# Kernel optimization log

Measured on AMD Instinct MI355X. Metric: run time of the kernel, lower is better.

Reference implementation:

```python
import jax, jax.numpy as jnp
import numpy as np

# Dims: C = 8*8*4 = 256 input channels, O = 8*8*8 = 512 output channels,
# space_rank = 4, TT ranks = (4, 16, 16).

def setup_inputs() -> dict:
    key = jax.random.key(0)
    ks = jax.random.split(key, 6)
    inp = jax.random.normal(ks[0], (32, 256, 32, 32), dtype=jnp.float32)
    # space_factor: (space_rank, 1, kH, kW)
    space_factor = jax.random.normal(ks[1], (4, 1, 3, 3), dtype=jnp.float32) * 0.3
    # factors[i]: (in_i, rank_i, rank_{i+1}, out_i)
    factor0 = jax.random.normal(ks[2], (8, 4, 16, 8), dtype=jnp.float32) * 0.1
    factor1 = jax.random.normal(ks[3], (8, 16, 16, 8), dtype=jnp.float32) * 0.08
    # last_factor: (in_last, rank_last, out_last)
    last_factor = jax.random.normal(ks[4], (4, 16, 8), dtype=jnp.float32) * 0.1
    bias = jax.random.uniform(ks[5], (512,), dtype=jnp.float32, minval=-0.02, maxval=0.02)
    return {"input": inp, "space_factor": space_factor, "factor0": factor0,
            "factor1": factor1, "last_factor": last_factor, "bias": bias}


def reference(input, space_factor, factor0, factor1, last_factor, bias):
    B, C, H, W = input.shape
    sr = space_factor.shape[0]
    # Depthwise conv: each of the C channels convolved with the same
    # `space_rank` filters (torch repeat along out-channel dim + groups=C).
    w = jnp.tile(space_factor, (C, 1, 1, 1))  # (C*sr, 1, kH, kW)
    y = jax.lax.conv_general_dilated(
        input, w, window_strides=(1, 1), padding=[(1, 1), (1, 1)],
        feature_group_count=C,
        dimension_numbers=("NCHW", "OIHW", "NCHW"))  # (B, C*sr, H', W')
    Hp, Wp = y.shape[2], y.shape[3]
    # (B, n0, n1, n2, sr, H', W') with (n0,n1,n2) = input_chanel_shape
    t = y.reshape(B, 8, 8, 4, sr, Hp, Wp)
    # Contract the tiny TT cores first (optimal order found by tn.contractors.optimal):
    # chain: (n0, n1, n2, r0, o0, o1, o2) -- only ~0.5M elements.
    chain = jnp.einsum("apqx,bqry,crz->abcpxyz", factor0, factor1, last_factor)
    # One big contraction over (n0, n1, n2, r0): effectively a GEMM
    # (B*H'*W', C*sr) x (C*sr, O).
    out = jnp.einsum("nabcphw,abcpxyz->nxyzhw", t, chain)
    out = out.reshape(B, 512, Hp, Wp)
    return out + bias[None, :, None, None]
```

## Files before the change

kernel.cpp:

```cpp
#include <hip/hip_runtime.h>

typedef unsigned short ushort_t;
typedef __attribute__((ext_vector_type(8))) short bf16x8;
typedef __attribute__((ext_vector_type(4))) float f32x4;

__device__ __forceinline__ unsigned short f2bf(float f) {
  union { float f; unsigned u; } x; x.f = f;
  unsigned r = x.u + 0x7FFFu + ((x.u >> 16) & 1u);
  return (unsigned short)(r >> 16);
}

__global__ void chain_g_kernel(const float* __restrict__ f1,
                               const float* __restrict__ lf,
                               float* __restrict__ g) {
  int idx = blockIdx.x * 256 + threadIdx.x;
  int z = idx & 7, c = (idx >> 3) & 3, y = (idx >> 5) & 7,
      q = (idx >> 8) & 15, b = idx >> 12;
  float s = 0.f;
  #pragma unroll
  for (int r = 0; r < 16; ++r)
    s += f1[((b * 16 + q) * 16 + r) * 8 + y] * lf[(c * 16 + r) * 8 + z];
  g[idx] = s;
}

__global__ void chain_kernel(const float* __restrict__ f0,
                             const float* __restrict__ g,
                             ushort_t* __restrict__ chainT) {
  int idx = blockIdx.x * 256 + threadIdx.x;
  int k = idx & 1023, o = idx >> 10;
  int p = k & 3, c = (k >> 2) & 3, b = (k >> 4) & 7, a = k >> 7;
  int z = o & 7, y = (o >> 3) & 7, x = o >> 6;
  float s = 0.f;
  #pragma unroll
  for (int q = 0; q < 16; ++q)
    s += f0[((a * 4 + p) * 16 + q) * 8 + x] *
         g[(((b * 16 + q) * 8 + y) * 4 + c) * 8 + z];
  chainT[idx] = f2bf(s);
}

#define AS1 __attribute__((address_space(1)))
#define AS3 __attribute__((address_space(3)))
#define BARRIER  __builtin_amdgcn_s_barrier()
#define LGKMCNT0 asm volatile("s_waitcnt lgkmcnt(0)" ::: "memory")
#define VMCNT3   asm volatile("s_waitcnt vmcnt(3)" ::: "memory")
#define VMCNT0   asm volatile("s_waitcnt vmcnt(0)" ::: "memory")

__global__ __launch_bounds__(512, 2) void fused_kernel(const float* __restrict__ in,
                                                       const float* __restrict__ sf,
                                                       const ushort_t* __restrict__ chainT,
                                                       const float* __restrict__ bias,
                                                       float* __restrict__ out) {
  __shared__ __align__(16) ushort_t Bs[32768];
  __shared__ __align__(16) ushort_t As[2][8192];
  __shared__ __align__(16) float Is[6528];

  int tid = threadIdx.x;
  int bid = blockIdx.x;
  int wg = (bid & 7) * 32 + (bid >> 3);
  int n = wg >> 3, hq = wg & 7;
  int h0 = hq * 4;

  int lane = tid & 63, wv = tid >> 6;
  int wm = (wv >> 2) * 64, wn = (wv & 3) * 128;
  int lr = lane & 15, kg = lane >> 4;
  int kph0 = ((kg * 8) ^ ((lane & 7) * 8));
  int kph1 = ((32 + kg * 8) ^ ((lane & 7) * 8));

  int srow = tid >> 3;
  int scol = ((tid & 7) ^ (srow & 7)) * 8;
  const ushort_t* sB = chainT + (size_t)srow * 1024 + scol;

  int cw = tid & 31, hp = (tid >> 5) & 1, ch2 = wv;
  int clm = (cw == 0) ? 33 : cw - 1;
  int crp = (cw == 31) ? 32 : cw + 1;
  int aswz = (ch2 ^ (cw & 7)) * 8;

  int isrc[3], ild[3], izer[3];
  #pragma unroll
  for (int i = 0; i < 3; ++i) {
    int e = tid + i * 512;
    int ch = e / 96, rem = e % 96, r = rem >> 4, w2 = rem & 15;
    int hh = h0 - 1 + r;
    int hcl = hh < 0 ? 0 : (hh > 31 ? 31 : hh);
    izer[i] = (hh < 0) | (hh > 31);
    isrc[i] = ch * 1024 + hcl * 32 + w2 * 2;
    ild[i]  = ch * 204 + r * 34 + w2 * 2;
  }
  const float* inb = in + (size_t)n * 262144;
  float2 rin[3];

  float sfr[36];
  #pragma unroll
  for (int i = 0; i < 36; ++i)
    sfr[i] = __int_as_float(__builtin_amdgcn_readfirstlane(__float_as_int(sf[i])));

  float bv[8];
  #pragma unroll
  for (int nf = 0; nf < 8; ++nf) bv[nf] = bias[wn + nf * 16 + lr];

  f32x4 acc[4][8];
  #pragma unroll
  for (int i = 0; i < 4; ++i)
    #pragma unroll
    for (int j = 0; j < 8; ++j) acc[i][j] = (f32x4){0.f, 0.f, 0.f, 0.f};

#define ISSUE_IN(KT)                                                                     \
  _Pragma("unroll")                                                                      \
  for (int i = 0; i < 3; ++i)                                                            \
    rin[i] = *(const float2*)&inb[(size_t)(KT) * 16384 + isrc[i]];

#define WRITE_IN(IB)                                                                     \
  _Pragma("unroll")                                                                      \
  for (int i = 0; i < 3; ++i) {                                                          \
    float2 v = rin[i];                                                                   \
    if (izer[i]) { v.x = 0.f; v.y = 0.f; }                                               \
    *(float2*)&Is[(IB) * 3264 + ild[i]] = v;                                             \
  }

#define STAGE_B(KT)                                                                      \
  _Pragma("unroll")                                                                      \
  for (int l = 0; l < 8; ++l)                                                            \
    __builtin_amdgcn_global_load_lds(                                                    \
        (const AS1 void*)(sB + (size_t)l * 65536 + (KT) * 64),                           \
        (AS3 void*)&Bs[l * 4096 + tid * 8], 16, 0, 0);

#define CONV(IB, AB)                                                                     \
  {                                                                                      \
    float tap[2][4][3];                                                                  \
    _Pragma("unroll")                                                                    \
    for (int b = 0; b < 2; ++b) {                                                        \
      const float* isp = &Is[(IB) * 3264 + (ch2 * 2 + b) * 204];                         \
      _Pragma("unroll")                                                                  \
      for (int r4 = 0; r4 < 4; ++r4) {                                                   \
        int rb = (hp * 2 + r4) * 34;                                                     \
        tap[b][r4][0] = isp[rb + clm];                                                   \
        tap[b][r4][1] = isp[rb + cw];                                                    \
        tap[b][r4][2] = isp[rb + crp];                                                   \
      }                                                                                  \
    }                                                                                    \
    _Pragma("unroll")                                                                    \
    for (int j = 0; j < 2; ++j) {                                                        \
      unsigned pw[4];                                                                    \
      _Pragma("unroll")                                                                  \
      for (int b = 0; b < 2; ++b) {                                                      \
        float s[4];                                                                      \
        _Pragma("unroll")                                                                \
        for (int p = 0; p < 4; ++p) {                                                    \
          float a_ = 0.f;                                                                \
          _Pragma("unroll")                                                              \
          for (int dr = 0; dr < 3; ++dr)                                                 \
            _Pragma("unroll")                                                            \
            for (int dt = 0; dt < 3; ++dt)                                               \
              a_ += tap[b][j + dr][dt] * sfr[p * 9 + dr * 3 + dt];                       \
          s[p] = a_;                                                                     \
        }                                                                                \
        pw[b * 2 + 0] = (unsigned)f2bf(s[0]) | ((unsigned)f2bf(s[1]) << 16);             \
        pw[b * 2 + 1] = (unsigned)f2bf(s[2]) | ((unsigned)f2bf(s[3]) << 16);             \
      }                                                                                  \
      uint4 pk; pk.x = pw[0]; pk.y = pw[1]; pk.z = pw[2]; pk.w = pw[3];                  \
      int row = (hp * 2 + j) * 32 + cw;                                                  \
      *(uint4*)&As[AB][row * 64 + aswz] = pk;                                            \
    }                                                                                    \
  }

#define MFMA_PHASE(AB)                                                                   \
  _Pragma("unroll")                                                                      \
  for (int ks = 0; ks < 2; ++ks) {                                                       \
    int kph = ks ? kph1 : kph0;                                                          \
    bf16x8 af[4];                                                                        \
    _Pragma("unroll")                                                                    \
    for (int mf = 0; mf < 4; ++mf)                                                       \
      af[mf] = *(const bf16x8*)&As[AB][(wm + mf * 16 + lr) * 64 + kph];                  \
    _Pragma("unroll")                                                                    \
    for (int ng = 0; ng < 2; ++ng) {                                                     \
      bf16x8 bq[4];                                                                      \
      _Pragma("unroll")                                                                  \
      for (int nq = 0; nq < 4; ++nq)                                                     \
        bq[nq] = *(const bf16x8*)&Bs[(wn + ng * 64 + nq * 16 + lr) * 64 + kph];          \
      __builtin_amdgcn_s_setprio(1);                                                     \
      _Pragma("unroll")                                                                  \
      for (int mf = 0; mf < 4; ++mf)                                                     \
        _Pragma("unroll")                                                                \
        for (int nq = 0; nq < 4; ++nq)                                                   \
          acc[mf][ng * 4 + nq] = __builtin_amdgcn_mfma_f32_16x16x32_bf16(                \
              af[mf], bq[nq], acc[mf][ng * 4 + nq], 0, 0, 0);                            \
      __builtin_amdgcn_s_setprio(0);                                                     \
    }                                                                                    \
  }

  if (tid < 384) {
    int bb = tid / 192, rem = tid % 192, ch = rem / 12, rr = rem % 12;
    Is[bb * 3264 + ch * 204 + (rr >> 1) * 34 + 32 + (rr & 1)] = 0.f;
  }
  ISSUE_IN(0)
  WRITE_IN(0)
  ISSUE_IN(1)
  LGKMCNT0; BARRIER;
  CONV(0, 0)
  WRITE_IN(1)
  STAGE_B(0)
  ISSUE_IN(2)
  LGKMCNT0; VMCNT3; BARRIER;

  #pragma unroll 1
  for (int I = 0; I < 8; ++I) {
    MFMA_PHASE(0)
    CONV(1, 1)
    if (I < 7) { WRITE_IN(0) }
    LGKMCNT0; BARRIER;
    STAGE_B(2 * I + 1)
    if (I < 7) { ISSUE_IN(2 * I + 3) VMCNT3; } else { VMCNT0; }
    BARRIER;
    MFMA_PHASE(1)
    if (I < 7) { CONV(0, 0) WRITE_IN(1) }
    LGKMCNT0; BARRIER;
    if (I < 7) {
      STAGE_B(2 * I + 2)
      if (I < 6) { ISSUE_IN(2 * I + 4) VMCNT3; } else { VMCNT0; }
    }
    BARRIER;
  }

  #pragma unroll
  for (int mf = 0; mf < 4; ++mf)
    #pragma unroll
    for (int nf = 0; nf < 8; ++nf) {
      int mloc = hq * 128 + wm + mf * 16 + kg * 4;
      int o = wn + nf * 16 + lr;
      f32x4 vv = acc[mf][nf];
      vv[0] += bv[nf]; vv[1] += bv[nf]; vv[2] += bv[nf]; vv[3] += bv[nf];
      *(f32x4*)&out[(size_t)n * 524288 + (size_t)o * 1024 + mloc] = vv;
    }
}

extern "C" void kernel_launch(void* const* d_in, const int* in_sizes, int n_in,
                              void* d_out, int out_size, void* d_ws, size_t ws_size,
                              hipStream_t stream) {
  (void)in_sizes; (void)n_in; (void)out_size; (void)ws_size;
  const float* in   = (const float*)d_in[0];
  const float* sf   = (const float*)d_in[1];
  const float* f0   = (const float*)d_in[2];
  const float* f1   = (const float*)d_in[3];
  const float* lf   = (const float*)d_in[4];
  const float* bias = (const float*)d_in[5];
  float* out = (float*)d_out;

  char* ws = (char*)d_ws;
  ushort_t* chainT = (ushort_t*)ws;
  float*    g      = (float*)(ws + 1048576);

  hipLaunchKernelGGL(chain_g_kernel, dim3(128),  dim3(256), 0, stream, f1, lf, g);
  hipLaunchKernelGGL(chain_kernel,   dim3(2048), dim3(256), 0, stream, f0, g, chainT);
  hipLaunchKernelGGL(fused_kernel,   dim3(256),  dim3(512), 0, stream, in, sf, chainT, bias, out);
}
```

Baseline: 74.21 us.

## Split output channels across two workgroups to raise occupancy and grid size

Each workgroup now computes half of the 512 output channels, so the grid doubles to 512 blocks and the accumulator and B tile shrink by half. Launch bounds ask for 4 blocks per CU, and the input staging buffer is single-buffered and unpadded, with edge zeros handled in registers. This is meant to fill the 256 CUs better and hide latency with more resident waves. In exchange the depthwise conv is recomputed twice per pixel tile, there are more barriers per iteration, and the single input buffer serializes conv and staging.

```diff
diff --git a/kernel.cpp b/kernel.cpp
--- a/kernel.cpp
+++ b/kernel.cpp
@@ -45,34 +45,32 @@
 #define VMCNT3   asm volatile("s_waitcnt vmcnt(3)" ::: "memory")
 #define VMCNT0   asm volatile("s_waitcnt vmcnt(0)" ::: "memory")
 
-__global__ __launch_bounds__(512, 2) void fused_kernel(const float* __restrict__ in,
+__global__ __launch_bounds__(512, 4) void fused_kernel(const float* __restrict__ in,
                                                        const float* __restrict__ sf,
                                                        const ushort_t* __restrict__ chainT,
                                                        const float* __restrict__ bias,
                                                        float* __restrict__ out) {
-  __shared__ __align__(16) ushort_t Bs[32768];
+  __shared__ __align__(16) ushort_t Bs[16384];
   __shared__ __align__(16) ushort_t As[2][8192];
-  __shared__ __align__(16) float Is[6528];
+  __shared__ __align__(16) float Is[3072];
 
   int tid = threadIdx.x;
   int bid = blockIdx.x;
-  int wg = (bid & 7) * 32 + (bid >> 3);
-  int n = wg >> 3, hq = wg & 7;
-  int h0 = hq * 4;
+  int wg = (bid & 7) * 64 + (bid >> 3);
+  int pix = wg >> 1, nh = wg & 1;
+  int n = pix >> 3, hq = pix & 7, h0 = hq * 4;
 
   int lane = tid & 63, wv = tid >> 6;
-  int wm = (wv >> 2) * 64, wn = (wv & 3) * 128;
+  int wm = (wv >> 2) * 64, wn = (wv & 3) * 64;
   int lr = lane & 15, kg = lane >> 4;
   int kph0 = ((kg * 8) ^ ((lane & 7) * 8));
   int kph1 = ((32 + kg * 8) ^ ((lane & 7) * 8));
 
   int srow = tid >> 3;
   int scol = ((tid & 7) ^ (srow & 7)) * 8;
-  const ushort_t* sB = chainT + (size_t)srow * 1024 + scol;
+  const ushort_t* sB = chainT + (size_t)(nh * 256 + srow) * 1024 + scol;
 
   int cw = tid & 31, hp = (tid >> 5) & 1, ch2 = wv;
-  int clm = (cw == 0) ? 33 : cw - 1;
-  int crp = (cw == 31) ? 32 : cw + 1;
   int aswz = (ch2 ^ (cw & 7)) * 8;
 
   int isrc[3], ild[3], izer[3];
@@ -84,7 +82,7 @@
     int hcl = hh < 0 ? 0 : (hh > 31 ? 31 : hh);
     izer[i] = (hh < 0) | (hh > 31);
     isrc[i] = ch * 1024 + hcl * 32 + w2 * 2;
-    ild[i]  = ch * 204 + r * 34 + w2 * 2;
+    ild[i]  = ch * 192 + r * 32 + w2 * 2;
   }
   const float* inb = in + (size_t)n * 262144;
   float2 rin[3];
@@ -94,70 +92,73 @@
   for (int i = 0; i < 36; ++i)
     sfr[i] = __int_as_float(__builtin_amdgcn_readfirstlane(__float_as_int(sf[i])));
 
-  float bv[8];
-  #pragma unroll
-  for (int nf = 0; nf < 8; ++nf) bv[nf] = bias[wn + nf * 16 + lr];
-
-  f32x4 acc[4][8];
+  float bv[4];
+  #pragma unroll
+  for (int nf = 0; nf < 4; ++nf) bv[nf] = bias[nh * 256 + wn + nf * 16 + lr];
+
+  f32x4 acc[4][4];
   #pragma unroll
   for (int i = 0; i < 4; ++i)
     #pragma unroll
-    for (int j = 0; j < 8; ++j) acc[i][j] = (f32x4){0.f, 0.f, 0.f, 0.f};
+    for (int j = 0; j < 4; ++j) acc[i][j] = (f32x4){0.f, 0.f, 0.f, 0.f};
 
 #define ISSUE_IN(KT)                                                                     \
   _Pragma("unroll")                                                                      \
   for (int i = 0; i < 3; ++i)                                                            \
     rin[i] = *(const float2*)&inb[(size_t)(KT) * 16384 + isrc[i]];
 
-#define WRITE_IN(IB)                                                                     \
+#define WRITE_IN                                                                         \
   _Pragma("unroll")                                                                      \
   for (int i = 0; i < 3; ++i) {                                                          \
     float2 v = rin[i];                                                                   \
     if (izer[i]) { v.x = 0.f; v.y = 0.f; }                                               \
-    *(float2*)&Is[(IB) * 3264 + ild[i]] = v;                                             \
+    *(float2*)&Is[ild[i]] = v;                                                           \
   }
 
 #define STAGE_B(KT)                                                                      \
   _Pragma("unroll")                                                                      \
-  for (int l = 0; l < 8; ++l)                                                            \
+  for (int l = 0; l < 4; ++l)                                                            \
     __builtin_amdgcn_global_load_lds(                                                    \
         (const AS1 void*)(sB + (size_t)l * 65536 + (KT) * 64),                           \
         (AS3 void*)&Bs[l * 4096 + tid * 8], 16, 0, 0);
 
-#define CONV(IB, AB)                                                                     \
+#define CONV(AB)                                                                         \
   {                                                                                      \
-    float tap[2][4][3];                                                                  \
+    unsigned pw[2][4];                                                                   \
     _Pragma("unroll")                                                                    \
     for (int b = 0; b < 2; ++b) {                                                        \
-      const float* isp = &Is[(IB) * 3264 + (ch2 * 2 + b) * 204];                         \
+      const float* isp = &Is[(ch2 * 2 + b) * 192];                                       \
+      float tap[4][3];                                                                   \
       _Pragma("unroll")                                                                  \
       for (int r4 = 0; r4 < 4; ++r4) {                                                   \
-        int rb = (hp * 2 + r4) * 34;                                                     \
-        tap[b][r4][0] = isp[rb + clm];                                                   \
-        tap[b][r4][1] = isp[rb + cw];                                                    \
-        tap[b][r4][2] = isp[rb + crp];                                                   \
+        int rb = (hp * 2 + r4) * 32;                                                     \
+        float lv = isp[rb + ((cw == 0) ? 0 : cw - 1)];                                   \
+        float mv = isp[rb + cw];                                                         \
+        float rv = isp[rb + ((cw == 31) ? 31 : cw + 1)];                                 \
+        tap[r4][0] = (cw == 0) ? 0.f : lv;                                               \
+        tap[r4][1] = mv;                                                                 \
+        tap[r4][2] = (cw == 31) ? 0.f : rv;                                              \
+      }                                                                                  \
+      _Pragma("unroll")                                                                  \
+      for (int j = 0; j < 2; ++j) {                                                      \
+        float s0 = 0.f, s1 = 0.f, s2 = 0.f, s3 = 0.f;                                    \
+        _Pragma("unroll")                                                                \
+        for (int dr = 0; dr < 3; ++dr)                                                   \
+          _Pragma("unroll")                                                              \
+          for (int dt = 0; dt < 3; ++dt) {                                               \
+            float tv = tap[j + dr][dt];                                                  \
+            s0 += tv * sfr[0 * 9 + dr * 3 + dt];                                         \
+            s1 += tv * sfr[1 * 9 + dr * 3 + dt];                                         \
+            s2 += tv * sfr[2 * 9 + dr * 3 + dt];                                         \
+            s3 += tv * sfr[3 * 9 + dr * 3 + dt];                                         \
+          }                                                                              \
+        pw[j][b * 2 + 0] = (unsigned)f2bf(s0) | ((unsigned)f2bf(s1) << 16);              \
+        pw[j][b * 2 + 1] = (unsigned)f2bf(s2) | ((unsigned)f2bf(s3) << 16);              \
       }                                                                                  \
     }                                                                                    \
     _Pragma("unroll")                                                                    \
     for (int j = 0; j < 2; ++j) {                                                        \
-      unsigned pw[4];                                                                    \
-      _Pragma("unroll")                                                                  \
-      for (int b = 0; b < 2; ++b) {                                                      \
-        float s[4];                                                                      \
-        _Pragma("unroll")                                                                \
-        for (int p = 0; p < 4; ++p) {                                                    \
-          float a_ = 0.f;                                                                \
-          _Pragma("unroll")                                                              \
-          for (int dr = 0; dr < 3; ++dr)                                                 \
-            _Pragma("unroll")                                                            \
-            for (int dt = 0; dt < 3; ++dt)                                               \
-              a_ += tap[b][j + dr][dt] * sfr[p * 9 + dr * 3 + dt];                       \
-          s[p] = a_;                                                                     \
-        }                                                                                \
-        pw[b * 2 + 0] = (unsigned)f2bf(s[0]) | ((unsigned)f2bf(s[1]) << 16);             \
-        pw[b * 2 + 1] = (unsigned)f2bf(s[2]) | ((unsigned)f2bf(s[3]) << 16);             \
-      }                                                                                  \
-      uint4 pk; pk.x = pw[0]; pk.y = pw[1]; pk.z = pw[2]; pk.w = pw[3];                  \
+      uint4 pk; pk.x = pw[j][0]; pk.y = pw[j][1]; pk.z = pw[j][2]; pk.w = pw[j][3];      \
       int row = (hp * 2 + j) * 32 + cw;                                                  \
       *(uint4*)&As[AB][row * 64 + aswz] = pk;                                            \
     }                                                                                    \
@@ -167,66 +168,62 @@
   _Pragma("unroll")                                                                      \
   for (int ks = 0; ks < 2; ++ks) {                                                       \
     int kph = ks ? kph1 : kph0;                                                          \
-    bf16x8 af[4];                                                                        \
+    bf16x8 af[4], bq[4];                                                                 \
     _Pragma("unroll")                                                                    \
     for (int mf = 0; mf < 4; ++mf)                                                       \
       af[mf] = *(const bf16x8*)&As[AB][(wm + mf * 16 + lr) * 64 + kph];                  \
     _Pragma("unroll")                                                                    \
-    for (int ng = 0; ng < 2; ++ng) {                                                     \
-      bf16x8 bq[4];                                                                      \
+    for (int nq = 0; nq < 4; ++nq)                                                       \
+      bq[nq] = *(const bf16x8*)&Bs[(wn + nq * 16 + lr) * 64 + kph];                      \
+    __builtin_amdgcn_s_setprio(1);                                                       \
+    _Pragma("unroll")                                                                    \
+    for (int mf = 0; mf < 4; ++mf)                                                       \
       _Pragma("unroll")                                                                  \
       for (int nq = 0; nq < 4; ++nq)                                                     \
-        bq[nq] = *(const bf16x8*)&Bs[(wn + ng * 64 + nq * 16 + lr) * 64 + kph];          \
-      __builtin_amdgcn_s_setprio(1);                                                     \
-      _Pragma("unroll")                                                                  \
-      for (int mf = 0; mf < 4; ++mf)                                                     \
-        _Pragma("unroll")                                                                \
-        for (int nq = 0; nq < 4; ++nq)                                                   \
-          acc[mf][ng * 4 + nq] = __builtin_amdgcn_mfma_f32_16x16x32_bf16(                \
-              af[mf], bq[nq], acc[mf][ng * 4 + nq], 0, 0, 0);                            \
-      __builtin_amdgcn_s_setprio(0);                                                     \
-    }                                                                                    \
-  }
-
-  if (tid < 384) {
-    int bb = tid / 192, rem = tid % 192, ch = rem / 12, rr = rem % 12;
-    Is[bb * 3264 + ch * 204 + (rr >> 1) * 34 + 32 + (rr & 1)] = 0.f;
-  }
+        acc[mf][nq] = __builtin_amdgcn_mfma_f32_16x16x32_bf16(                           \
+            af[mf], bq[nq], acc[mf][nq], 0, 0, 0);                                       \
+    __builtin_amdgcn_s_setprio(0);                                                       \
+  }
+
   ISSUE_IN(0)
-  WRITE_IN(0)
+  WRITE_IN
   ISSUE_IN(1)
   LGKMCNT0; BARRIER;
-  CONV(0, 0)
-  WRITE_IN(1)
+  CONV(0)
   STAGE_B(0)
+  LGKMCNT0; BARRIER;
+  WRITE_IN
   ISSUE_IN(2)
   LGKMCNT0; VMCNT3; BARRIER;
 
   #pragma unroll 1
   for (int I = 0; I < 8; ++I) {
     MFMA_PHASE(0)
-    CONV(1, 1)
-    if (I < 7) { WRITE_IN(0) }
     LGKMCNT0; BARRIER;
     STAGE_B(2 * I + 1)
-    if (I < 7) { ISSUE_IN(2 * I + 3) VMCNT3; } else { VMCNT0; }
+    CONV(1)
+    LGKMCNT0; BARRIER;
+    if (I < 7) { WRITE_IN ISSUE_IN(2 * I + 3) }
+    LGKMCNT0;
+    if (I < 7) { VMCNT3; } else { VMCNT0; }
     BARRIER;
     MFMA_PHASE(1)
-    if (I < 7) { CONV(0, 0) WRITE_IN(1) }
-    LGKMCNT0; BARRIER;
-    if (I < 7) {
-      STAGE_B(2 * I + 2)
-      if (I < 6) { ISSUE_IN(2 * I + 4) VMCNT3; } else { VMCNT0; }
-    }
+    LGKMCNT0; BARRIER;
+    if (I < 7) { STAGE_B(2 * I + 2) CONV(0) }
+    LGKMCNT0; BARRIER;
+    if (I < 7) { WRITE_IN }
+    if (I < 6) { ISSUE_IN(2 * I + 4) }
+    LGKMCNT0;
+    if (I < 6) { VMCNT3; } else { VMCNT0; }
     BARRIER;
   }
 
   #pragma unroll
   for (int mf = 0; mf < 4; ++mf)
     #pragma unroll
-    for (int nf = 0; nf < 8; ++nf) {
+    for (int nf = 0; nf < 4; ++nf) {
       int mloc = hq * 128 + wm + mf * 16 + kg * 4;
-      int o = wn + nf * 16 + lr;
+      int o = nh * 256 + wn + nf * 16 + lr;
       f32x4 vv = acc[mf][nf];
       vv[0] += bv[nf]; vv[1] += bv[nf]; vv[2] += bv[nf]; vv[3] += bv[nf];
       *(f32x4*)&out[(size_t)n * 524288 + (size_t)o * 1024 + mloc] = vv;
@@ -251,5 +248,5 @@
 
   hipLaunchKernelGGL(chain_g_kernel, dim3(128),  dim3(256), 0, stream, f1, lf, g);
   hipLaunchKernelGGL(chain_kernel,   dim3(2048), dim3(256), 0, stream, f0, g, chainT);
-  hipLaunchKernelGGL(fused_kernel,   dim3(256),  dim3(512), 0, stream, in, sf, chainT, bias, out);
-}
+  hipLaunchKernelGGL(fused_kernel,   dim3(512),  dim3(512), 0, stream, in, sf, chainT, bias, out);
+}
```

Result: slower. 109.4 us (+47.4%).
